# Optimization experiments

Measured on AMD Instinct MI355X. Metric: run time of the kernel, lower is better.

## Reference

```python
import jax, jax.numpy as jnp
import numpy as np

BATCH = 8192
IN_F = 1024
OUT_F = 1024
GRID_SIZE = 5
SPLINE_ORDER = 3
GRID_LO, GRID_HI = -1.0, 1.0


def setup_inputs() -> dict:
    key = jax.random.key(0)
    k1, k2, k3, k4 = jax.random.split(key, 4)
    x = jax.random.normal(k1, (BATCH, IN_F), dtype=jnp.float32)
    # grid buffer: extended knot vector, same for every input feature
    h = (GRID_HI - GRID_LO) / GRID_SIZE
    knots = jnp.linspace(GRID_LO - SPLINE_ORDER * h, GRID_HI + SPLINE_ORDER * h,
                         GRID_SIZE + 2 * SPLINE_ORDER + 1, dtype=jnp.float32)
    grid = jnp.tile(knots[None, :], (IN_F, 1))  # [in, 12]
    fan_in_scale = 1.0 / np.sqrt(IN_F)
    base_weight = jax.random.normal(k2, (OUT_F, IN_F), dtype=jnp.float32) * fan_in_scale
    spline_weight = jax.random.normal(k3, (IN_F, GRID_SIZE + SPLINE_ORDER, OUT_F), dtype=jnp.float32) * 0.1
    spline_scaler = jax.random.normal(k4, (IN_F, OUT_F), dtype=jnp.float32) * fan_in_scale
    return {"x": x, "grid": grid, "base_weight": base_weight,
            "spline_weight": spline_weight, "spline_scaler": spline_scaler}


def b_splines(x, grid):
    """Cox-de Boor recursion. x: [B, in], grid: [in, G+2k+1] -> [B, in, G+k]."""
    xe = x[:, :, None]  # [B, in, 1]
    bases = ((xe >= grid[:, :-1]) & (xe < grid[:, 1:])).astype(x.dtype)  # [B, in, G+2k]
    for k in range(1, SPLINE_ORDER + 1):
        left = (xe - grid[:, :-(k + 1)]) / (grid[:, k:-1] - grid[:, :-(k + 1)])
        right = (grid[:, k + 1:] - xe) / (grid[:, k + 1:] - grid[:, 1:-k])
        bases = left * bases[:, :, :-1] + right * bases[:, :, 1:]
    return bases  # [B, in, G+k]


def reference(x, grid, base_weight, spline_weight, spline_scaler):
    # base branch: SiLU(x) @ W_base^T
    base_out = jax.nn.silu(x) @ base_weight.T  # [B, out]
    # spline branch
    basis = b_splines(x, grid)  # [B, in, G+k]
    scaled_w = spline_weight * spline_scaler[:, None, :]  # [in, G+k, out]
    spline_out = jnp.einsum('bik,iko->bo', basis, scaled_w)  # [B, out]
    return base_out + spline_out
```

## Files before the change

kernel.cpp:

```cpp
#include <hip/hip_runtime.h>
#include <cstdint>
#include <cstddef>

#define BATCH 8192
#define IN_F 1024
#define OUT_F 1024
#define NSPL 9
#define KDIM (IN_F * NSPL)

typedef __bf16 bf16x8 __attribute__((ext_vector_type(8)));
typedef float f32x4 __attribute__((ext_vector_type(4)));

__device__ __forceinline__ void g2l16(const void* g, void* l) {
  __builtin_amdgcn_global_load_lds(
      (__attribute__((address_space(1))) void*)(g),
      (__attribute__((address_space(3))) void*)(l),
      16, 0, 0);
}

__global__ void build_w(const float* __restrict__ bw, const float* __restrict__ sw,
                        const float* __restrict__ sc, __bf16* __restrict__ Wt) {
  __shared__ float s_sw[16 * 8 * 64];
  __shared__ float s_sc[16 * 64];
  __shared__ float s_bw[64 * 16];
  const int tid = threadIdx.x;
  const int o0 = (blockIdx.x & 15) * 64;
  const int i0 = (blockIdx.x >> 4) * 16;

#pragma unroll
  for (int it = 0; it < 32; ++it) {
    const int t = it * 256 + tid;
    const int i = t >> 9, r = (t >> 6) & 7, oo = t & 63;
    s_sw[t] = sw[((size_t)(i0 + i) * 8 + r) * OUT_F + o0 + oo];
  }
#pragma unroll
  for (int it = 0; it < 4; ++it) {
    const int t = it * 256 + tid;
    const int i = t >> 6, oo = t & 63;
    s_sc[t] = sc[(size_t)(i0 + i) * OUT_F + o0 + oo];
  }
#pragma unroll
  for (int it = 0; it < 4; ++it) {
    const int t = it * 256 + tid;
    const int oo = t >> 4, ii = t & 15;
    s_bw[t] = bw[(size_t)(o0 + oo) * IN_F + i0 + ii];
  }
  __syncthreads();

  const int oo = tid >> 2;
  const int isub = (tid & 3) * 4;
#pragma unroll
  for (int is = 0; is < 4; ++is) {
    const int i = isub + is;
    __bf16* dst = Wt + (size_t)(o0 + oo) * KDIM + (size_t)(i0 + i) * NSPL;
    dst[0] = (__bf16)s_bw[oo * 16 + i];
    const float scal = s_sc[i * 64 + oo];
#pragma unroll
    for (int r = 0; r < 8; ++r)
      dst[1 + r] = (__bf16)(s_sw[i * 512 + r * 64 + oo] * scal);
  }
}

__global__ void build_a(const float* __restrict__ x, __bf16* __restrict__ A) {
  __shared__ __align__(16) __bf16 rowbuf[KDIM];
  const int b = blockIdx.x;
  const int tid = threadIdx.x;
#pragma unroll
  for (int c = 0; c < IN_F / 256; ++c) {
    const int i = c * 256 + tid;
    const float v = x[(size_t)b * IN_F + i];
    float w[NSPL];
#pragma unroll
    for (int r = 0; r < NSPL; ++r) w[r] = 0.f;
    w[0] = v / (1.f + __expf(-v));
    const float p = (v + 2.2f) * 2.5f;
    const int cell = (int)floorf(p);
    if (cell >= 0 && cell <= 10 && v < 2.2f) {
      const float t = p - (float)cell;
      const float t2 = t * t, t3 = t2 * t;
      const float omt = 1.f - t;
      const float b0 = (1.f / 6.f) * omt * omt * omt;
      const float b1 = (1.f / 6.f) * (3.f * t3 - 6.f * t2 + 4.f);
      const float b2 = (1.f / 6.f) * (-3.f * t3 + 3.f * t2 + 3.f * t + 1.f);
      const float b3 = (1.f / 6.f) * t3;
      const int j0 = cell - 3;
      if (j0 + 0 >= 0 && j0 + 0 <= 7) w[1 + j0 + 0] = b0;
      if (j0 + 1 >= 0 && j0 + 1 <= 7) w[1 + j0 + 1] = b1;
      if (j0 + 2 >= 0 && j0 + 2 <= 7) w[1 + j0 + 2] = b2;
      if (j0 + 3 >= 0 && j0 + 3 <= 7) w[1 + j0 + 3] = b3;
    }
    __bf16* d = rowbuf + (size_t)i * NSPL;
#pragma unroll
    for (int r = 0; r < NSPL; ++r) d[r] = (__bf16)w[r];
  }
  __syncthreads();
  const uint4* src = (const uint4*)rowbuf;
  uint4* dst = (uint4*)(A + (size_t)b * KDIM);
  for (int t = tid; t < KDIM * 2 / 16; t += 256)
    dst[t] = src[t];
}

__global__ __launch_bounds__(256) void gemm_bt(const __bf16* __restrict__ A,
                                               const __bf16* __restrict__ W,
                                               float* __restrict__ out) {
  __shared__ __align__(16) __bf16 As[2 * 128 * 32];
  __shared__ __align__(16) __bf16 Bs[2 * 128 * 32];

  const int tid = threadIdx.x;
  const int wv = tid >> 6;
  const int lane = tid & 63;
  const int mb = blockIdx.x & 63;
  const int nb = blockIdx.x >> 6;
  const int m0 = mb * 128;
  const int n0 = nb * 128;
  const int wr = wv & 1;
  const int wc = wv >> 1;

  const int srow = lane >> 2;
  const int scol = (lane & 3) * 8;
  const __bf16* gA = A + (size_t)(m0 + wv * 32 + srow) * KDIM + scol;
  const __bf16* gB = W + (size_t)(n0 + wv * 32 + srow) * KDIM + scol;
  __bf16* lA = As + wv * 1024;
  __bf16* lB = Bs + wv * 1024;

  const int mrow = lane & 15;
  const int quad = lane >> 4;
  int aoff[4], boff[4];
#pragma unroll
  for (int mt = 0; mt < 4; ++mt) aoff[mt] = (wr * 64 + mt * 16 + mrow) * 32 + quad * 8;
#pragma unroll
  for (int nt = 0; nt < 4; ++nt) boff[nt] = (wc * 64 + nt * 16 + mrow) * 32 + quad * 8;

  f32x4 acc[4][4];
  const f32x4 zero = {0.f, 0.f, 0.f, 0.f};
#pragma unroll
  for (int mt = 0; mt < 4; ++mt)
#pragma unroll
    for (int nt = 0; nt < 4; ++nt) acc[mt][nt] = zero;

  for (int k0 = 0; k0 < KDIM; k0 += 64) {
    __syncthreads();
    g2l16(gA + k0, lA);
    g2l16(gA + k0 + (size_t)16 * KDIM, lA + 512);
    g2l16(gB + k0, lB);
    g2l16(gB + k0 + (size_t)16 * KDIM, lB + 512);
    g2l16(gA + k0 + 32, lA + 4096);
    g2l16(gA + k0 + 32 + (size_t)16 * KDIM, lA + 4096 + 512);
    g2l16(gB + k0 + 32, lB + 4096);
    g2l16(gB + k0 + 32 + (size_t)16 * KDIM, lB + 4096 + 512);
    __syncthreads();

    bf16x8 af[2][4], bfr[2][4];
#pragma unroll
    for (int h = 0; h < 2; ++h) {
#pragma unroll
      for (int mt = 0; mt < 4; ++mt) af[h][mt] = *(const bf16x8*)(As + h * 4096 + aoff[mt]);
#pragma unroll
      for (int nt = 0; nt < 4; ++nt) bfr[h][nt] = *(const bf16x8*)(Bs + h * 4096 + boff[nt]);
    }
#pragma unroll
    for (int h = 0; h < 2; ++h)
#pragma unroll
      for (int mt = 0; mt < 4; ++mt)
#pragma unroll
        for (int nt = 0; nt < 4; ++nt)
          acc[mt][nt] = __builtin_amdgcn_mfma_f32_16x16x32_bf16(af[h][mt], bfr[h][nt],
                                                                acc[mt][nt], 0, 0, 0);
  }

#pragma unroll
  for (int mt = 0; mt < 4; ++mt) {
#pragma unroll
    for (int nt = 0; nt < 4; ++nt) {
      const int col = n0 + wc * 64 + nt * 16 + mrow;
      const int rbase = m0 + wr * 64 + mt * 16 + quad * 4;
#pragma unroll
      for (int r = 0; r < 4; ++r)
        out[(size_t)(rbase + r) * OUT_F + col] = acc[mt][nt][r];
    }
  }
}

extern "C" void kernel_launch(void* const* d_in, const int* in_sizes, int n_in,
                              void* d_out, int out_size, void* d_ws, size_t ws_size,
                              hipStream_t stream) {
  const float* x  = (const float*)d_in[0];
  const float* bw = (const float*)d_in[2];
  const float* sw = (const float*)d_in[3];
  const float* sc = (const float*)d_in[4];
  float* out = (float*)d_out;

  __bf16* Wt = (__bf16*)d_ws;
  __bf16* Ab = (__bf16*)((char*)d_ws +
                         (size_t)OUT_F * KDIM * sizeof(__bf16));

  build_w<<<1024, 256, 0, stream>>>(bw, sw, sc, Wt);
  build_a<<<BATCH, 256, 0, stream>>>(x, Ab);
  gemm_bt<<<(BATCH / 128) * (OUT_F / 128), 256, 0, stream>>>(Ab, Wt, out);
}
```

Baseline: 313.8 us.

## Split GEMM K dimension in two with atomic accumulation and merge prep kernels

Fuses the weight-building and activation-building kernels into one launch that dispatches on block index. Splits the GEMM reduction dimension into two halves, doubling the block count from 512 to 1024 so the GPU's compute units are better filled, and accumulates the partial results with float atomics into an output that is zeroed first by a memset. In exchange it adds a full output memset, doubles the output write traffic through atomics, and makes the summation order nondeterministic.

```diff
diff --git a/kernel.cpp b/kernel.cpp
--- a/kernel.cpp
+++ b/kernel.cpp
@@ -7,6 +7,8 @@
 #define OUT_F 1024
 #define NSPL 9
 #define KDIM (IN_F * NSPL)
+#define KSPLIT 2
+#define KHALF (KDIM / KSPLIT)
 
 typedef __bf16 bf16x8 __attribute__((ext_vector_type(8)));
 typedef float f32x4 __attribute__((ext_vector_type(4)));
@@ -18,86 +20,91 @@
       16, 0, 0);
 }
 
-__global__ void build_w(const float* __restrict__ bw, const float* __restrict__ sw,
-                        const float* __restrict__ sc, __bf16* __restrict__ Wt) {
-  __shared__ float s_sw[16 * 8 * 64];
-  __shared__ float s_sc[16 * 64];
-  __shared__ float s_bw[64 * 16];
+__global__ __launch_bounds__(256) void prep(const float* __restrict__ x,
+                                            const float* __restrict__ bw,
+                                            const float* __restrict__ sw,
+                                            const float* __restrict__ sc,
+                                            __bf16* __restrict__ Wt,
+                                            __bf16* __restrict__ Ab) {
+  __shared__ __align__(16) char smem[40960];
   const int tid = threadIdx.x;
-  const int o0 = (blockIdx.x & 15) * 64;
-  const int i0 = (blockIdx.x >> 4) * 16;
-
-#pragma unroll
-  for (int it = 0; it < 32; ++it) {
-    const int t = it * 256 + tid;
-    const int i = t >> 9, r = (t >> 6) & 7, oo = t & 63;
-    s_sw[t] = sw[((size_t)(i0 + i) * 8 + r) * OUT_F + o0 + oo];
+
+  if (blockIdx.x < 1024) {
+    float* s_sw = (float*)smem;
+    float* s_sc = (float*)(smem + 32768);
+    float* s_bw = (float*)(smem + 36864);
+    const int o0 = (blockIdx.x & 15) * 64;
+    const int i0 = (blockIdx.x >> 4) * 16;
+
+#pragma unroll
+    for (int it = 0; it < 32; ++it) {
+      const int t = it * 256 + tid;
+      const int i = t >> 9, r = (t >> 6) & 7, oo = t & 63;
+      s_sw[t] = sw[((size_t)(i0 + i) * 8 + r) * OUT_F + o0 + oo];
+    }
+#pragma unroll
+    for (int it = 0; it < 4; ++it) {
+      const int t = it * 256 + tid;
+      const int i = t >> 6, oo = t & 63;
+      s_sc[t] = sc[(size_t)(i0 + i) * OUT_F + o0 + oo];
+    }
+#pragma unroll
+    for (int it = 0; it < 4; ++it) {
+      const int t = it * 256 + tid;
+      const int oo = t >> 4, ii = t & 15;
+      s_bw[t] = bw[(size_t)(o0 + oo) * IN_F + i0 + ii];
+    }
+    __syncthreads();
+
+    const int oo = tid >> 2;
+    const int isub = (tid & 3) * 4;
+#pragma unroll
+    for (int is = 0; is < 4; ++is) {
+      const int i = isub + is;
+      __bf16* dst = Wt + (size_t)(o0 + oo) * KDIM + (size_t)(i0 + i) * NSPL;
+      dst[0] = (__bf16)s_bw[oo * 16 + i];
+      const float scal = s_sc[i * 64 + oo];
+#pragma unroll
+      for (int r = 0; r < 8; ++r)
+        dst[1 + r] = (__bf16)(s_sw[i * 512 + r * 64 + oo] * scal);
+    }
+  } else {
+    __bf16* rowbuf = (__bf16*)smem;
+    const int b = blockIdx.x - 1024;
+#pragma unroll
+    for (int c = 0; c < IN_F / 256; ++c) {
+      const int i = c * 256 + tid;
+      const float v = x[(size_t)b * IN_F + i];
+      float w[NSPL];
+#pragma unroll
+      for (int r = 0; r < NSPL; ++r) w[r] = 0.f;
+      w[0] = v / (1.f + __expf(-v));
+      const float p = (v + 2.2f) * 2.5f;
+      const int cell = (int)floorf(p);
+      if (cell >= 0 && cell <= 10 && v < 2.2f) {
+        const float t = p - (float)cell;
+        const float t2 = t * t, t3 = t2 * t;
+        const float omt = 1.f - t;
+        const float b0 = (1.f / 6.f) * omt * omt * omt;
+        const float b1 = (1.f / 6.f) * (3.f * t3 - 6.f * t2 + 4.f);
+        const float b2 = (1.f / 6.f) * (-3.f * t3 + 3.f * t2 + 3.f * t + 1.f);
+        const float b3 = (1.f / 6.f) * t3;
+        const int j0 = cell - 3;
+        if (j0 + 0 >= 0 && j0 + 0 <= 7) w[1 + j0 + 0] = b0;
+        if (j0 + 1 >= 0 && j0 + 1 <= 7) w[1 + j0 + 1] = b1;
+        if (j0 + 2 >= 0 && j0 + 2 <= 7) w[1 + j0 + 2] = b2;
+        if (j0 + 3 >= 0 && j0 + 3 <= 7) w[1 + j0 + 3] = b3;
+      }
+      __bf16* d = rowbuf + (size_t)i * NSPL;
+#pragma unroll
+      for (int r = 0; r < NSPL; ++r) d[r] = (__bf16)w[r];
+    }
+    __syncthreads();
+    const uint4* src = (const uint4*)rowbuf;
+    uint4* dst = (uint4*)(Ab + (size_t)b * KDIM);
+    for (int t = tid; t < KDIM * 2 / 16; t += 256)
+      dst[t] = src[t];
   }
-#pragma unroll
-  for (int it = 0; it < 4; ++it) {
-    const int t = it * 256 + tid;
-    const int i = t >> 6, oo = t & 63;
-    s_sc[t] = sc[(size_t)(i0 + i) * OUT_F + o0 + oo];
-  }
-#pragma unroll
-  for (int it = 0; it < 4; ++it) {
-    const int t = it * 256 + tid;
-    const int oo = t >> 4, ii = t & 15;
-    s_bw[t] = bw[(size_t)(o0 + oo) * IN_F + i0 + ii];
-  }
-  __syncthreads();
-
-  const int oo = tid >> 2;
-  const int isub = (tid & 3) * 4;
-#pragma unroll
-  for (int is = 0; is < 4; ++is) {
-    const int i = isub + is;
-    __bf16* dst = Wt + (size_t)(o0 + oo) * KDIM + (size_t)(i0 + i) * NSPL;
-    dst[0] = (__bf16)s_bw[oo * 16 + i];
-    const float scal = s_sc[i * 64 + oo];
-#pragma unroll
-    for (int r = 0; r < 8; ++r)
-      dst[1 + r] = (__bf16)(s_sw[i * 512 + r * 64 + oo] * scal);
-  }
-}
-
-__global__ void build_a(const float* __restrict__ x, __bf16* __restrict__ A) {
-  __shared__ __align__(16) __bf16 rowbuf[KDIM];
-  const int b = blockIdx.x;
-  const int tid = threadIdx.x;
-#pragma unroll
-  for (int c = 0; c < IN_F / 256; ++c) {
-    const int i = c * 256 + tid;
-    const float v = x[(size_t)b * IN_F + i];
-    float w[NSPL];
-#pragma unroll
-    for (int r = 0; r < NSPL; ++r) w[r] = 0.f;
-    w[0] = v / (1.f + __expf(-v));
-    const float p = (v + 2.2f) * 2.5f;
-    const int cell = (int)floorf(p);
-    if (cell >= 0 && cell <= 10 && v < 2.2f) {
-      const float t = p - (float)cell;
-      const float t2 = t * t, t3 = t2 * t;
-      const float omt = 1.f - t;
-      const float b0 = (1.f / 6.f) * omt * omt * omt;
-      const float b1 = (1.f / 6.f) * (3.f * t3 - 6.f * t2 + 4.f);
-      const float b2 = (1.f / 6.f) * (-3.f * t3 + 3.f * t2 + 3.f * t + 1.f);
-      const float b3 = (1.f / 6.f) * t3;
-      const int j0 = cell - 3;
-      if (j0 + 0 >= 0 && j0 + 0 <= 7) w[1 + j0 + 0] = b0;
-      if (j0 + 1 >= 0 && j0 + 1 <= 7) w[1 + j0 + 1] = b1;
-      if (j0 + 2 >= 0 && j0 + 2 <= 7) w[1 + j0 + 2] = b2;
-      if (j0 + 3 >= 0 && j0 + 3 <= 7) w[1 + j0 + 3] = b3;
-    }
-    __bf16* d = rowbuf + (size_t)i * NSPL;
-#pragma unroll
-    for (int r = 0; r < NSPL; ++r) d[r] = (__bf16)w[r];
-  }
-  __syncthreads();
-  const uint4* src = (const uint4*)rowbuf;
-  uint4* dst = (uint4*)(A + (size_t)b * KDIM);
-  for (int t = tid; t < KDIM * 2 / 16; t += 256)
-    dst[t] = src[t];
 }
 
 __global__ __launch_bounds__(256) void gemm_bt(const __bf16* __restrict__ A,
@@ -109,17 +116,20 @@
   const int tid = threadIdx.x;
   const int wv = tid >> 6;
   const int lane = tid & 63;
-  const int mb = blockIdx.x & 63;
-  const int nb = blockIdx.x >> 6;
+  const int ks = blockIdx.x >> 9;
+  const int b2 = blockIdx.x & 511;
+  const int mb = b2 & 63;
+  const int nb = b2 >> 6;
   const int m0 = mb * 128;
   const int n0 = nb * 128;
+  const int kbase = ks * KHALF;
   const int wr = wv & 1;
   const int wc = wv >> 1;
 
   const int srow = lane >> 2;
   const int scol = (lane & 3) * 8;
-  const __bf16* gA = A + (size_t)(m0 + wv * 32 + srow) * KDIM + scol;
-  const __bf16* gB = W + (size_t)(n0 + wv * 32 + srow) * KDIM + scol;
+  const __bf16* gA = A + (size_t)(m0 + wv * 32 + srow) * KDIM + scol + kbase;
+  const __bf16* gB = W + (size_t)(n0 + wv * 32 + srow) * KDIM + scol + kbase;
   __bf16* lA = As + wv * 1024;
   __bf16* lB = Bs + wv * 1024;
 
@@ -138,7 +148,7 @@
 #pragma unroll
     for (int nt = 0; nt < 4; ++nt) acc[mt][nt] = zero;
 
-  for (int k0 = 0; k0 < KDIM; k0 += 64) {
+  for (int k0 = 0; k0 < KHALF; k0 += 64) {
     __syncthreads();
     g2l16(gA + k0, lA);
     g2l16(gA + k0 + (size_t)16 * KDIM, lA + 512);
@@ -176,7 +186,7 @@
       const int rbase = m0 + wr * 64 + mt * 16 + quad * 4;
 #pragma unroll
       for (int r = 0; r < 4; ++r)
-        out[(size_t)(rbase + r) * OUT_F + col] = acc[mt][nt][r];
+        unsafeAtomicAdd(&out[(size_t)(rbase + r) * OUT_F + col], acc[mt][nt][r]);
     }
   }
 }
@@ -194,7 +204,7 @@
   __bf16* Ab = (__bf16*)((char*)d_ws +
                          (size_t)OUT_F * KDIM * sizeof(__bf16));
 
-  build_w<<<1024, 256, 0, stream>>>(bw, sw, sc, Wt);
-  build_a<<<BATCH, 256, 0, stream>>>(x, Ab);
-  gemm_bt<<<(BATCH / 128) * (OUT_F / 128), 256, 0, stream>>>(Ab, Wt, out);
-}
+  hipMemsetAsync(out, 0, (size_t)BATCH * OUT_F * sizeof(float), stream);
+  prep<<<1024 + BATCH, 256, 0, stream>>>(x, bw, sw, sc, Wt, Ab);
+  gemm_bt<<<KSPLIT * (BATCH / 128) * (OUT_F / 128), 256, 0, stream>>>(Ab, Wt, out);
+}
```

After: 387.5 us. +23.5%, slower.
